# Kernel tuning notes

Hardware: AMD Instinct MI355X
Metric: run time of the kernel (lower is better)

Reference implementation:

```python
import jax, jax.numpy as jnp
import numpy as np

H = 1024   # hidden_size
S = 32768  # seq_len


def setup_inputs() -> dict:
    key = jax.random.key(0)
    k1, k2, k3, k4 = jax.random.split(key, 4)
    scale = 1.0 / np.sqrt(H)
    return {
        "hidden": jax.random.normal(k1, (H,), dtype=jnp.float32),
        "encoder_outputs": jax.random.normal(k2, (S, H), dtype=jnp.float32),
        "W": jax.random.normal(k3, (H, H), dtype=jnp.float32) * scale,
        "b": jax.random.normal(k4, (H,), dtype=jnp.float32) * scale,
    }


def reference(hidden, encoder_outputs, W, b):
    # method == 'general': energy_i = W @ enc_i + b ; score_i = hidden . energy_i
    # Vectorized: scores = (enc @ W^T + b) @ hidden  -> [S]
    energies = jnp.einsum("sh,dh->sd", encoder_outputs, W) + b  # [S, H]
    scores = energies @ hidden                                   # [S]
    attn = jax.nn.softmax(scores)                                 # softmax over seq_len
    return attn[None, None, :]                                    # [1, 1, S]
```

## Files before the change

kernel.cpp:

```cpp
#include <hip/hip_runtime.h>
#include <math.h>

#define H 1024
#define S 32768
#define NPART 16

#define WS_PART   0
#define WS_SCORES 16384
#define WS_PM     (16384 + S)
#define WS_PS     (16384 + S + 1024)
#define WS_V      (16384 + S + 2048)

__global__ __launch_bounds__(256) void matvec_partial(const float* __restrict__ W,
                                                      const float* __restrict__ hidden,
                                                      float* __restrict__ ws) {
    float* part = ws + WS_PART;
    const int t  = threadIdx.x;
    const int l  = t & 63;
    const int dg = t >> 6;
    const int h  = blockIdx.x * 64 + l;
    const int d0 = blockIdx.y * 64 + dg * 16;

    float acc = 0.f;
#pragma unroll
    for (int i = 0; i < 16; ++i) {
        const int d = d0 + i;
        acc += W[(size_t)d * H + h] * hidden[d];
    }

    __shared__ float red[4][64];
    red[dg][l] = acc;
    __syncthreads();
    if (t < 64) {
        part[blockIdx.y * H + blockIdx.x * 64 + l] =
            red[0][l] + red[1][l] + red[2][l] + red[3][l];
    }
}

__global__ __launch_bounds__(64) void reduce_v(float* __restrict__ ws) {
    const float* part = ws + WS_PART;
    float* v = ws + WS_V;
    const int i = blockIdx.x * 64 + threadIdx.x;
    const float4* p4 = (const float4*)part;
    float4 a = p4[i];
#pragma unroll
    for (int p = 1; p < NPART; ++p) {
        const float4 w = p4[p * (H / 4) + i];
        a.x += w.x; a.y += w.y; a.z += w.z; a.w += w.w;
    }
    ((float4*)v)[i] = a;
}

__global__ __launch_bounds__(256) void scores_partial(const float* __restrict__ enc,
                                                      float* __restrict__ ws) {
    float* scores = ws + WS_SCORES;
    float* pm     = ws + WS_PM;
    float* ps     = ws + WS_PS;
    const float* v = ws + WS_V;

    const int tid  = threadIdx.x;
    const int lane = tid & 63;
    const int wv   = tid >> 6;
    const int blk  = blockIdx.x;
    const int gw   = blk * 4 + wv;
    const size_t row0 = (size_t)gw * 8;

    const float4* v4 = (const float4*)v;
    float4 vf[4];
#pragma unroll
    for (int k = 0; k < 4; ++k) vf[k] = v4[lane + 64 * k];

    float a[8];
#pragma unroll
    for (int it = 0; it < 8; ++it) {
        const float4* e4 = (const float4*)(enc + (row0 + it) * H);
        const float4 e0 = e4[lane];
        const float4 e1 = e4[lane + 64];
        const float4 e2 = e4[lane + 128];
        const float4 e3 = e4[lane + 192];
        float s0 = e0.x * vf[0].x + e0.y * vf[0].y + e0.z * vf[0].z + e0.w * vf[0].w;
        float s1 = e1.x * vf[1].x + e1.y * vf[1].y + e1.z * vf[1].z + e1.w * vf[1].w;
        float s2 = e2.x * vf[2].x + e2.y * vf[2].y + e2.z * vf[2].z + e2.w * vf[2].w;
        float s3 = e3.x * vf[3].x + e3.y * vf[3].y + e3.z * vf[3].z + e3.w * vf[3].w;
        a[it] = (s0 + s1) + (s2 + s3);
    }

#pragma unroll
    for (int it = 0; it < 8; ++it) {
#pragma unroll
        for (int off = 32; off > 0; off >>= 1)
            a[it] += __shfl_xor(a[it], off, 64);
        if (lane == 0) scores[row0 + it] = a[it];
    }

    float m01 = fmaxf(a[0], a[1]), m23 = fmaxf(a[2], a[3]);
    float m45 = fmaxf(a[4], a[5]), m67 = fmaxf(a[6], a[7]);
    const float mw = fmaxf(fmaxf(m01, m23), fmaxf(m45, m67));
    float sw = 0.f;
#pragma unroll
    for (int it = 0; it < 8; ++it) sw += __expf(a[it] - mw);

    __shared__ float sm[4], ss[4];
    if (lane == 0) { sm[wv] = mw; ss[wv] = sw; }
    __syncthreads();
    if (tid == 0) {
        float m = sm[0], s = ss[0];
#pragma unroll
        for (int i = 1; i < 4; ++i) {
            const float nm = fmaxf(m, sm[i]);
            s = s * __expf(m - nm) + ss[i] * __expf(sm[i] - nm);
            m = nm;
        }
        pm[blk] = m; ps[blk] = s;
    }
}

__global__ __launch_bounds__(256) void finalize(const float* __restrict__ ws,
                                                float* __restrict__ out) {
    const float* scores = ws + WS_SCORES;
    const float* pm     = ws + WS_PM;
    const float* ps     = ws + WS_PS;

    const int tid  = threadIdx.x;
    const int lane = tid & 63;
    const int wv   = tid >> 6;

    float m = -INFINITY, s = 0.f;
#pragma unroll
    for (int i = 0; i < 4; ++i) {
        const int idx = tid + i * 256;
        const float om = pm[idx], os = ps[idx];
        const float nm = fmaxf(m, om);
        s = s * __expf(m - nm) + os * __expf(om - nm);
        m = nm;
    }
#pragma unroll
    for (int off = 32; off > 0; off >>= 1) {
        const float om = __shfl_xor(m, off, 64);
        const float os = __shfl_xor(s, off, 64);
        const float nm = fmaxf(m, om);
        s = s * __expf(m - nm) + os * __expf(om - nm);
        m = nm;
    }
    __shared__ float sm[4], ss[4];
    if (lane == 0) { sm[wv] = m; ss[wv] = s; }
    __syncthreads();
    float M = sm[0], Ssum = ss[0];
#pragma unroll
    for (int i = 1; i < 4; ++i) {
        const float nm = fmaxf(M, sm[i]);
        Ssum = Ssum * __expf(M - nm) + ss[i] * __expf(sm[i] - nm);
        M = nm;
    }
    const float rs = 1.0f / Ssum;

    const int i = blockIdx.x * 256 + tid;
    out[i] = __expf(scores[i] - M) * rs;
}

extern "C" void kernel_launch(void* const* d_in, const int* in_sizes, int n_in,
                              void* d_out, int out_size, void* d_ws, size_t ws_size,
                              hipStream_t stream) {
    const float* hidden = (const float*)d_in[0];
    const float* enc    = (const float*)d_in[1];
    const float* W      = (const float*)d_in[2];
    float* out = (float*)d_out;
    float* ws  = (float*)d_ws;

    matvec_partial<<<dim3(16, 16), 256, 0, stream>>>(W, hidden, ws);
    reduce_v<<<4, 64, 0, stream>>>(ws);
    scores_partial<<<1024, 256, 0, stream>>>(enc, ws);
    finalize<<<S / 256, 256, 0, stream>>>(ws, out);
}
```

Baseline: 203.5 us.

## Fuse all four attention stages into one persistent kernel with atomic grid barriers

Replaces the four launches (partial matvec, reduce, scores, finalize) with one 512-block kernel that uses atomic counters as grid-wide barriers. Each wave now handles 16 rows and prefetches its first two encoder rows before waiting on v. Scores stay in registers, so the scores array is never written to or read back from global memory. The design relies on all 512 blocks being co-resident, which launch_bounds(256,2) is meant to allow, and adds spin-wait latency plus a memset launch.

```diff
diff --git a/kernel.cpp b/kernel.cpp
--- a/kernel.cpp
+++ b/kernel.cpp
@@ -3,104 +3,128 @@
 
 #define H 1024
 #define S 32768
-#define NPART 16
+#define NBLK 512
+#define RPW 16
 
-#define WS_PART   0
-#define WS_SCORES 16384
-#define WS_PM     (16384 + S)
-#define WS_PS     (16384 + S + 1024)
-#define WS_V      (16384 + S + 2048)
+#define WS_PART 0
+#define WS_V    16384
+#define WS_PM   17408
+#define WS_PS   17920
+#define WS_CTR  18432
 
-__global__ __launch_bounds__(256) void matvec_partial(const float* __restrict__ W,
-                                                      const float* __restrict__ hidden,
-                                                      float* __restrict__ ws) {
-    float* part = ws + WS_PART;
-    const int t  = threadIdx.x;
-    const int l  = t & 63;
-    const int dg = t >> 6;
-    const int h  = blockIdx.x * 64 + l;
-    const int d0 = blockIdx.y * 64 + dg * 16;
+__device__ __forceinline__ float dot16(const float4 e0, const float4 e1,
+                                       const float4 e2, const float4 e3,
+                                       const float4 vf[4]) {
+    float s0 = e0.x * vf[0].x + e0.y * vf[0].y + e0.z * vf[0].z + e0.w * vf[0].w;
+    float s1 = e1.x * vf[1].x + e1.y * vf[1].y + e1.z * vf[1].z + e1.w * vf[1].w;
+    float s2 = e2.x * vf[2].x + e2.y * vf[2].y + e2.z * vf[2].z + e2.w * vf[2].w;
+    float s3 = e3.x * vf[3].x + e3.y * vf[3].y + e3.z * vf[3].z + e3.w * vf[3].w;
+    return (s0 + s1) + (s2 + s3);
+}
 
-    float acc = 0.f;
-#pragma unroll
-    for (int i = 0; i < 16; ++i) {
-        const int d = d0 + i;
-        acc += W[(size_t)d * H + h] * hidden[d];
-    }
-
-    __shared__ float red[4][64];
-    red[dg][l] = acc;
-    __syncthreads();
-    if (t < 64) {
-        part[blockIdx.y * H + blockIdx.x * 64 + l] =
-            red[0][l] + red[1][l] + red[2][l] + red[3][l];
+__device__ __forceinline__ void spin_until_ge(int* p, int target) {
+    int guard = 0;
+    while (__hip_atomic_load(p, __ATOMIC_RELAXED, __HIP_MEMORY_SCOPE_AGENT) < target) {
+        __builtin_amdgcn_s_sleep(2);
+        if (++guard > 20000000) break;
     }
 }
 
-__global__ __launch_bounds__(64) void reduce_v(float* __restrict__ ws) {
-    const float* part = ws + WS_PART;
-    float* v = ws + WS_V;
-    const int i = blockIdx.x * 64 + threadIdx.x;
-    const float4* p4 = (const float4*)part;
-    float4 a = p4[i];
-#pragma unroll
-    for (int p = 1; p < NPART; ++p) {
-        const float4 w = p4[p * (H / 4) + i];
-        a.x += w.x; a.y += w.y; a.z += w.z; a.w += w.w;
-    }
-    ((float4*)v)[i] = a;
-}
-
-__global__ __launch_bounds__(256) void scores_partial(const float* __restrict__ enc,
-                                                      float* __restrict__ ws) {
-    float* scores = ws + WS_SCORES;
-    float* pm     = ws + WS_PM;
-    float* ps     = ws + WS_PS;
-    const float* v = ws + WS_V;
+__global__ __launch_bounds__(256, 2) void attn_fused(const float* __restrict__ hidden,
+                                                     const float* __restrict__ enc,
+                                                     const float* __restrict__ W,
+                                                     float* __restrict__ ws,
+                                                     float* __restrict__ out) {
+    float* part = ws + WS_PART;
+    float* v    = ws + WS_V;
+    float* pm   = ws + WS_PM;
+    float* ps   = ws + WS_PS;
+    int*   ctr  = (int*)(ws + WS_CTR);
 
     const int tid  = threadIdx.x;
     const int lane = tid & 63;
     const int wv   = tid >> 6;
     const int blk  = blockIdx.x;
-    const int gw   = blk * 4 + wv;
-    const size_t row0 = (size_t)gw * 8;
+
+    __shared__ float red[4][64];
+    __shared__ float sm[4], ss[4];
+    __shared__ float outsh[64];
+
+    if (blk < 256) {
+        const int dg = tid >> 6;
+        const int h  = (blk & 15) * 64 + lane;
+        const int d0 = (blk >> 4) * 64 + dg * 16;
+        float acc = 0.f;
+#pragma unroll
+        for (int i = 0; i < 16; ++i)
+            acc += W[(size_t)(d0 + i) * H + h] * hidden[d0 + i];
+        red[dg][lane] = acc;
+        __syncthreads();
+        if (tid < 64)
+            part[(blk >> 4) * H + (blk & 15) * 64 + tid] =
+                red[0][tid] + red[1][tid] + red[2][tid] + red[3][tid];
+        __syncthreads();
+        if (tid == 0)
+            __hip_atomic_fetch_add(&ctr[0], 1, __ATOMIC_RELEASE, __HIP_MEMORY_SCOPE_AGENT);
+    }
+
+    if (blk == 0) {
+        if (tid == 0) spin_until_ge(&ctr[0], 256);
+        __syncthreads();
+        __threadfence();
+        const float4* p4 = (const float4*)part;
+        float4 a4 = p4[tid];
+#pragma unroll
+        for (int p = 1; p < 16; ++p) {
+            const float4 w4 = p4[p * 256 + tid];
+            a4.x += w4.x; a4.y += w4.y; a4.z += w4.z; a4.w += w4.w;
+        }
+        ((float4*)v)[tid] = a4;
+        __syncthreads();
+        if (tid == 0)
+            __hip_atomic_store(&ctr[1], 1, __ATOMIC_RELEASE, __HIP_MEMORY_SCOPE_AGENT);
+    }
+
+    const int gw = blk * 4 + wv;
+    const float4* e4 = (const float4*)enc + (size_t)gw * (RPW * (H / 4));
+
+    float4 p00 = e4[lane],       p01 = e4[lane + 64],
+           p02 = e4[lane + 128], p03 = e4[lane + 192];
+    float4 p10 = e4[256 + lane],       p11 = e4[256 + lane + 64],
+           p12 = e4[256 + lane + 128], p13 = e4[256 + lane + 192];
+
+    if (tid == 0) spin_until_ge(&ctr[1], 1);
+    __syncthreads();
+    __threadfence();
 
     const float4* v4 = (const float4*)v;
     float4 vf[4];
 #pragma unroll
     for (int k = 0; k < 4; ++k) vf[k] = v4[lane + 64 * k];
 
-    float a[8];
+    float a[RPW];
+    a[0] = dot16(p00, p01, p02, p03, vf);
+    a[1] = dot16(p10, p11, p12, p13, vf);
 #pragma unroll
-    for (int it = 0; it < 8; ++it) {
-        const float4* e4 = (const float4*)(enc + (row0 + it) * H);
-        const float4 e0 = e4[lane];
-        const float4 e1 = e4[lane + 64];
-        const float4 e2 = e4[lane + 128];
-        const float4 e3 = e4[lane + 192];
-        float s0 = e0.x * vf[0].x + e0.y * vf[0].y + e0.z * vf[0].z + e0.w * vf[0].w;
-        float s1 = e1.x * vf[1].x + e1.y * vf[1].y + e1.z * vf[1].z + e1.w * vf[1].w;
-        float s2 = e2.x * vf[2].x + e2.y * vf[2].y + e2.z * vf[2].z + e2.w * vf[2].w;
-        float s3 = e3.x * vf[3].x + e3.y * vf[3].y + e3.z * vf[3].z + e3.w * vf[3].w;
-        a[it] = (s0 + s1) + (s2 + s3);
+    for (int it = 2; it < RPW; ++it) {
+        const float4* r = e4 + it * 256;
+        a[it] = dot16(r[lane], r[lane + 64], r[lane + 128], r[lane + 192], vf);
     }
 
 #pragma unroll
-    for (int it = 0; it < 8; ++it) {
+    for (int it = 0; it < RPW; ++it) {
 #pragma unroll
         for (int off = 32; off > 0; off >>= 1)
             a[it] += __shfl_xor(a[it], off, 64);
-        if (lane == 0) scores[row0 + it] = a[it];
     }
 
-    float m01 = fmaxf(a[0], a[1]), m23 = fmaxf(a[2], a[3]);
-    float m45 = fmaxf(a[4], a[5]), m67 = fmaxf(a[6], a[7]);
-    const float mw = fmaxf(fmaxf(m01, m23), fmaxf(m45, m67));
+    float mw = a[0];
+#pragma unroll
+    for (int it = 1; it < RPW; ++it) mw = fmaxf(mw, a[it]);
     float sw = 0.f;
 #pragma unroll
-    for (int it = 0; it < 8; ++it) sw += __expf(a[it] - mw);
+    for (int it = 0; it < RPW; ++it) sw += __expf(a[it] - mw);
 
-    __shared__ float sm[4], ss[4];
     if (lane == 0) { sm[wv] = mw; ss[wv] = sw; }
     __syncthreads();
     if (tid == 0) {
@@ -112,24 +136,17 @@
             m = nm;
         }
         pm[blk] = m; ps[blk] = s;
+        __hip_atomic_fetch_add(&ctr[2], 1, __ATOMIC_RELEASE, __HIP_MEMORY_SCOPE_AGENT);
     }
-}
 
-__global__ __launch_bounds__(256) void finalize(const float* __restrict__ ws,
-                                                float* __restrict__ out) {
-    const float* scores = ws + WS_SCORES;
-    const float* pm     = ws + WS_PM;
-    const float* ps     = ws + WS_PS;
-
-    const int tid  = threadIdx.x;
-    const int lane = tid & 63;
-    const int wv   = tid >> 6;
+    if (tid == 0) spin_until_ge(&ctr[2], NBLK);
+    __syncthreads();
+    __threadfence();
 
     float m = -INFINITY, s = 0.f;
 #pragma unroll
-    for (int i = 0; i < 4; ++i) {
-        const int idx = tid + i * 256;
-        const float om = pm[idx], os = ps[idx];
+    for (int i = 0; i < 2; ++i) {
+        const float om = pm[tid + i * 256], os = ps[tid + i * 256];
         const float nm = fmaxf(m, om);
         s = s * __expf(m - nm) + os * __expf(om - nm);
         m = nm;
@@ -142,7 +159,7 @@
         s = s * __expf(m - nm) + os * __expf(om - nm);
         m = nm;
     }
-    __shared__ float sm[4], ss[4];
+    __syncthreads();
     if (lane == 0) { sm[wv] = m; ss[wv] = s; }
     __syncthreads();
     float M = sm[0], Ssum = ss[0];
@@ -154,8 +171,13 @@
     }
     const float rs = 1.0f / Ssum;
 
-    const int i = blockIdx.x * 256 + tid;
-    out[i] = __expf(scores[i] - M) * rs;
+    if (lane == 0) {
+#pragma unroll
+        for (int it = 0; it < RPW; ++it)
+            outsh[wv * RPW + it] = __expf(a[it] - M) * rs;
+    }
+    __syncthreads();
+    if (tid < 64) out[blk * 64 + tid] = outsh[tid];
 }
 
 extern "C" void kernel_launch(void* const* d_in, const int* in_sizes, int n_in,
@@ -167,8 +189,6 @@
     float* out = (float*)d_out;
     float* ws  = (float*)d_ws;
 
-    matvec_partial<<<dim3(16, 16), 256, 0, stream>>>(W, hidden, ws);
-    reduce_v<<<4, 64, 0, stream>>>(ws);
-    scores_partial<<<1024, 256, 0, stream>>>(enc, ws);
-    finalize<<<S / 256, 256, 0, stream>>>(ws, out);
+    hipMemsetAsync((void*)(ws + WS_CTR), 0, 256, stream);
+    attn_fused<<<NBLK, 256, 0, stream>>>(hidden, enc, W, ws, out);
 }
```

Measured after the change: 317.8 us. +56.2%, slower.
